# Kernel optimization log

Hardware: AMD Instinct MI355X
Metric: run time of the kernel (lower is better)

## Reference

```python
import jax, jax.numpy as jnp
import numpy as np

B, N, D_IN, D_OUT, E = 2, 50000, 128, 64, 800000
NEG_SLOPE = 0.2  # LeakyReLU negative slope (alpha)


def setup_inputs() -> dict:
    key = jax.random.key(0)
    ks = jax.random.split(key, 8)
    X_key = jax.random.normal(ks[0], (B, N, D_IN), dtype=jnp.float32)
    X_value = jax.random.normal(ks[1], (B, N, D_IN), dtype=jnp.float32)
    src = jax.random.randint(ks[2], (E,), 0, N, dtype=jnp.int32)
    dst = jnp.sort(jax.random.randint(ks[3], (E,), 0, N, dtype=jnp.int32))
    s = 1.0 / np.sqrt(D_IN)
    Wk = jax.random.normal(ks[4], (D_IN, D_OUT), dtype=jnp.float32) * s
    bk = jnp.zeros((D_OUT,), dtype=jnp.float32)
    Wv = jax.random.normal(ks[5], (D_IN, D_OUT), dtype=jnp.float32) * s
    bv = jnp.zeros((D_OUT,), dtype=jnp.float32)
    return {"X_key": X_key, "X_value": X_value, "Wk": Wk, "bk": bk,
            "Wv": Wv, "bv": bv, "src": src, "dst": dst}


def reference(X_key, X_value, Wk, bk, Wv, bv, src, dst):
    n = X_key.shape[1]
    h_key = X_key @ Wk + bk      # [B, N, D_OUT]
    h_value = X_value @ Wv + bv  # [B, N, D_OUT]

    def per_batch(hk, hv):
        # per-edge dot-product attention score
        e = jnp.sum(hk[src] * hk[dst], axis=-1)                    # [E]
        m = jax.lax.stop_gradient(jax.ops.segment_max(e, dst, num_segments=n))
        a = jnp.exp(e - m[dst])                                    # [E]
        denom = jax.ops.segment_sum(a, dst, num_segments=n)        # [N]
        num = jax.ops.segment_sum(a[:, None] * hv[src], dst, num_segments=n)  # [N, D_OUT]
        # nodes with no incoming edges get 0 (DGL leaves them zero-initialized)
        return num / jnp.where(denom == 0, 1.0, denom)[:, None]

    h_att = jax.vmap(per_batch)(h_key, h_value)  # [B, N, D_OUT]
    # LeakyReLU(alpha=0.2)
    return jnp.where(h_att >= 0, h_att, NEG_SLOPE * h_att)
```

## Files before the change

kernel.cpp:

```cpp
#include <hip/hip_runtime.h>
#include <cfloat>
#include <math.h>

#define D_IN 128
#define D_OUT 64
#define NEG_SLOPE 0.2f
#define ROWH 128
#define SQRT_LOG2E 1.2011224087864498f

typedef _Float16 half2v __attribute__((ext_vector_type(2)));
typedef _Float16 half8 __attribute__((ext_vector_type(8)));
typedef float f32x4 __attribute__((ext_vector_type(4)));

__device__ __forceinline__ unsigned short f2bf(float x) {
  union { float f; unsigned u; } a; a.f = x;
  unsigned r = a.u + 0x7FFFu + ((a.u >> 16) & 1u);
  return (unsigned short)(r >> 16);
}
__device__ __forceinline__ unsigned short f2h(float x) {
  union { _Float16 h; unsigned short u; } c;
  c.h = (_Float16)x;
  return c.u;
}
__device__ __forceinline__ float4 unpack_bf4(uint2 q) {
  union { unsigned u; float f; } t;
  float4 r;
  t.u = q.x << 16;          r.x = t.f;
  t.u = q.x & 0xFFFF0000u;  r.y = t.f;
  t.u = q.y << 16;          r.z = t.f;
  t.u = q.y & 0xFFFF0000u;  r.w = t.f;
  return r;
}
__device__ __forceinline__ float hdot4(uint2 a, uint2 b) {
  union { unsigned u; half2v h; } al, ah, bl, bh;
  al.u = a.x; ah.u = a.y; bl.u = b.x; bh.u = b.y;
#if __has_builtin(__builtin_amdgcn_fdot2)
  return __builtin_amdgcn_fdot2(al.h, bl.h,
         __builtin_amdgcn_fdot2(ah.h, bh.h, 0.f, false), false);
#else
  return (float)al.h[0] * (float)bl.h[0] + (float)al.h[1] * (float)bl.h[1] +
         (float)ah.h[0] * (float)bh.h[0] + (float)ah.h[1] * (float)bh.h[1];
#endif
}

__global__ void bfrag_kernel(const float* __restrict__ Wk,
                             const float* __restrict__ Wv,
                             _Float16* __restrict__ bfrag) {
  const int idx = blockIdx.x * 256 + threadIdx.x;
  if (idx >= 2048) return;
  const int which = idx >> 10;
  const float* __restrict__ W = which ? Wv : Wk;
  const float scale = which ? 1.0f : SQRT_LOG2E;
  const int li = idx & 1023;
  const int lane = li & 63;
  const int nt = (li >> 6) & 3;
  const int k0i = li >> 8;
  const int col = nt * 16 + (lane & 15);
  const int kbase = k0i * 32 + (lane >> 4) * 8;
  half8 h;
#pragma unroll
  for (int j = 0; j < 8; ++j)
    h[j] = (_Float16)(W[(size_t)(kbase + j) * D_OUT + col] * scale);
  reinterpret_cast<half8*>(bfrag)[idx] = h;
}

__global__ __launch_bounds__(256) void linear_mfma_kernel(
    const float* __restrict__ Xk, const float* __restrict__ Xv,
    const float* __restrict__ Wk, const float* __restrict__ bk,
    const float* __restrict__ Wv, const float* __restrict__ bv,
    const _Float16* __restrict__ bfrag, unsigned short* __restrict__ hkv,
    int R, int nblk) {
  const int which = (blockIdx.x >= nblk) ? 1 : 0;
  const int blk = blockIdx.x - which * nblk;
  const float* __restrict__ X = which ? Xv : Xk;
  const float* __restrict__ bias = which ? bv : bk;
  const float bscale = which ? 1.0f : SQRT_LOG2E;
  const int uoff = which ? D_OUT : 0;

  const int wave = threadIdx.x >> 6;
  const int lane = threadIdx.x & 63;
  const int r0 = (blk * 4 + wave) * 16;
  if (r0 >= R) return;
  const int rowi = lane & 15;
  const int kgrp = lane >> 4;

  if (r0 + 16 <= R) {
    const half8* btab =
        reinterpret_cast<const half8*>(bfrag) + (which ? 1024 : 0);
    half8 bf[4][4];
#pragma unroll
    for (int k0i = 0; k0i < 4; ++k0i)
#pragma unroll
      for (int nt = 0; nt < 4; ++nt)
        bf[k0i][nt] = btab[(k0i * 4 + nt) * 64 + lane];

    f32x4 acc[4];
#pragma unroll
    for (int nt = 0; nt < 4; ++nt) acc[nt] = (f32x4){0.f, 0.f, 0.f, 0.f};

    const float* xrow = X + (size_t)(r0 + rowi) * D_IN;
#pragma unroll
    for (int k0i = 0; k0i < 4; ++k0i) {
      const float4 x0 =
          *reinterpret_cast<const float4*>(xrow + k0i * 32 + kgrp * 8);
      const float4 x1 =
          *reinterpret_cast<const float4*>(xrow + k0i * 32 + kgrp * 8 + 4);
      half8 a;
      a[0] = (_Float16)x0.x; a[1] = (_Float16)x0.y;
      a[2] = (_Float16)x0.z; a[3] = (_Float16)x0.w;
      a[4] = (_Float16)x1.x; a[5] = (_Float16)x1.y;
      a[6] = (_Float16)x1.z; a[7] = (_Float16)x1.w;
#pragma unroll
      for (int nt = 0; nt < 4; ++nt)
        acc[nt] = __builtin_amdgcn_mfma_f32_16x16x32_f16(a, bf[k0i][nt],
                                                         acc[nt], 0, 0, 0);
    }
#pragma unroll
    for (int nt = 0; nt < 4; ++nt) {
      const int col = nt * 16 + rowi;
      const float bcol = bias[col] * bscale;
#pragma unroll
      for (int r = 0; r < 4; ++r) {
        const int row = r0 + kgrp * 4 + r;
        const float val = acc[nt][r] + bcol;
        hkv[(size_t)row * ROWH + uoff + col] =
            which ? f2bf(val) : f2h(val);
      }
    }
  } else {
    const float* __restrict__ W = which ? Wv : Wk;
    for (int r = r0; r < R; ++r) {
      const float* xr = X + (size_t)r * D_IN;
      float acc = bias[lane];
      for (int k = 0; k < D_IN; ++k)
        acc = fmaf(xr[k], W[(size_t)k * D_OUT + lane], acc);
      acc *= bscale;
      hkv[(size_t)r * ROWH + uoff + lane] = which ? f2bf(acc) : f2h(acc);
    }
  }
}

__global__ void rowptr_kernel(const int* __restrict__ dst, int E, int N,
                              int* __restrict__ row_ptr) {
  int i = blockIdx.x * blockDim.x + threadIdx.x;
  if (i > N) return;
  int lo = 0, hi = E;
  while (lo < hi) {
    int mid = (lo + hi) >> 1;
    if (dst[mid] < i) lo = mid + 1; else hi = mid;
  }
  row_ptr[i] = lo;
}

__device__ __forceinline__ float rowsum16(float p) {
  union { float f; int i; } u, v;
  u.f = p;
  v.i = __builtin_amdgcn_update_dpp(0, u.i, 0x121, 0xF, 0xF, true);
  u.f += v.f;
  v.i = __builtin_amdgcn_update_dpp(0, u.i, 0x122, 0xF, 0xF, true);
  u.f += v.f;
  v.i = __builtin_amdgcn_update_dpp(0, u.i, 0x124, 0xF, 0xF, true);
  u.f += v.f;
  v.i = __builtin_amdgcn_update_dpp(0, u.i, 0x128, 0xF, 0xF, true);
  u.f += v.f;
  return u.f;
}

struct SMState { float m, l; float4 a; };

__device__ __forceinline__ void sm_update(SMState& st, float pl,
                                          const float4& vs) {
  if (pl > st.m) {
    const float sc = exp2f(st.m - pl);
    st.l *= sc;
    st.a.x *= sc; st.a.y *= sc; st.a.z *= sc; st.a.w *= sc;
    st.m = pl;
  }
  const float a = exp2f(pl - st.m);
  st.l += a;
  st.a.x = fmaf(a, vs.x, st.a.x);
  st.a.y = fmaf(a, vs.y, st.a.y);
  st.a.z = fmaf(a, vs.z, st.a.z);
  st.a.w = fmaf(a, vs.w, st.a.w);
}

__device__ __forceinline__ void sm_merge(SMState& d, const SMState& s) {
  const float mn = fmaxf(d.m, s.m);
  const float s1 = exp2f(d.m - mn);
  const float s2 = exp2f(s.m - mn);
  d.l = d.l * s1 + s.l * s2;
  d.a.x = d.a.x * s1 + s.a.x * s2;
  d.a.y = d.a.y * s1 + s.a.y * s2;
  d.a.z = d.a.z * s1 + s.a.z * s2;
  d.a.w = d.a.w * s1 + s.a.w * s2;
  d.m = mn;
}

__device__ __forceinline__ void sm_merge_xor(SMState& d, int off) {
  SMState s;
  s.m = __shfl_xor(d.m, off, 64);
  s.l = __shfl_xor(d.l, off, 64);
  s.a.x = __shfl_xor(d.a.x, off, 64);
  s.a.y = __shfl_xor(d.a.y, off, 64);
  s.a.z = __shfl_xor(d.a.z, off, 64);
  s.a.w = __shfl_xor(d.a.w, off, 64);
  sm_merge(d, s);
}

__global__ __launch_bounds__(256) void aggregate_kernel(
    const unsigned short* __restrict__ hkv, const int* __restrict__ src,
    const int* __restrict__ row_ptr, float* __restrict__ out, int N) {
  const int node = blockIdx.x * 4 + (threadIdx.x >> 6);
  const int lane = threadIdx.x & 63;
  if (node >= N) return;
  const unsigned short* hb0 = hkv;
  const unsigned short* hb1 = hkv + (size_t)N * ROWH;

  const int li = lane & 15;
  const int g = lane >> 4;

  const uint2 kd0 = reinterpret_cast<const uint2*>(hb0 + (size_t)node * ROWH)[li];
  const uint2 kd1 = reinterpret_cast<const uint2*>(hb1 + (size_t)node * ROWH)[li];
  const int e0 = row_ptr[node];
  const int e1 = row_ptr[node + 1];

  SMState A0 = {-FLT_MAX, 0.f, {0.f, 0.f, 0.f, 0.f}};
  SMState B0 = A0, A1 = A0, B1 = A0;

  int e = e0 + g;
  for (; e + 4 < e1; e += 8) {
    const int sA = src[e];
    const int sB = src[e + 4];
    const uint2* rA0 = reinterpret_cast<const uint2*>(hb0 + (size_t)sA * ROWH);
    const uint2* rA1 = reinterpret_cast<const uint2*>(hb1 + (size_t)sA * ROWH);
    const uint2* rB0 = reinterpret_cast<const uint2*>(hb0 + (size_t)sB * ROWH);
    const uint2* rB1 = reinterpret_cast<const uint2*>(hb1 + (size_t)sB * ROWH);
    const uint2 kA0 = rA0[li], vA0 = rA0[16 + li];
    const uint2 kA1 = rA1[li], vA1 = rA1[16 + li];
    const uint2 kB0 = rB0[li], vB0 = rB0[16 + li];
    const uint2 kB1 = rB1[li], vB1 = rB1[16 + li];

    const float plA0 = rowsum16(hdot4(kA0, kd0));
    const float plA1 = rowsum16(hdot4(kA1, kd1));
    const float plB0 = rowsum16(hdot4(kB0, kd0));
    const float plB1 = rowsum16(hdot4(kB1, kd1));

    sm_update(A0, plA0, unpack_bf4(vA0));
    sm_update(A1, plA1, unpack_bf4(vA1));
    sm_update(B0, plB0, unpack_bf4(vB0));
    sm_update(B1, plB1, unpack_bf4(vB1));
  }
  if (e < e1) {
    const int sA = src[e];
    const uint2* rA0 = reinterpret_cast<const uint2*>(hb0 + (size_t)sA * ROWH);
    const uint2* rA1 = reinterpret_cast<const uint2*>(hb1 + (size_t)sA * ROWH);
    const uint2 kA0 = rA0[li], vA0 = rA0[16 + li];
    const uint2 kA1 = rA1[li], vA1 = rA1[16 + li];
    const float plA0 = rowsum16(hdot4(kA0, kd0));
    const float plA1 = rowsum16(hdot4(kA1, kd1));
    sm_update(A0, plA0, unpack_bf4(vA0));
    sm_update(A1, plA1, unpack_bf4(vA1));
  }

  sm_merge(A0, B0);
  sm_merge(A1, B1);
  sm_merge_xor(A0, 16); sm_merge_xor(A0, 32);
  sm_merge_xor(A1, 16); sm_merge_xor(A1, 32);

  if (lane < 16) {
#pragma unroll
    for (int b = 0; b < 2; ++b) {
      const SMState& S = b ? A1 : A0;
      const float denom = (S.l == 0.f) ? 1.f : S.l;
      float4 o;
      o.x = S.a.x / denom; o.y = S.a.y / denom;
      o.z = S.a.z / denom; o.w = S.a.w / denom;
      o.x = (o.x >= 0.f) ? o.x : NEG_SLOPE * o.x;
      o.y = (o.y >= 0.f) ? o.y : NEG_SLOPE * o.y;
      o.z = (o.z >= 0.f) ? o.z : NEG_SLOPE * o.z;
      o.w = (o.w >= 0.f) ? o.w : NEG_SLOPE * o.w;
      *reinterpret_cast<float4*>(out + ((size_t)b * N + node) * D_OUT + 4 * lane) = o;
    }
  }
}

extern "C" void kernel_launch(void* const* d_in, const int* in_sizes, int n_in,
                              void* d_out, int out_size, void* d_ws,
                              size_t ws_size, hipStream_t stream) {
  const float* X_key   = (const float*)d_in[0];
  const float* X_value = (const float*)d_in[1];
  const float* Wk      = (const float*)d_in[2];
  const float* bk      = (const float*)d_in[3];
  const float* Wv      = (const float*)d_in[4];
  const float* bv      = (const float*)d_in[5];
  const int*   src     = (const int*)d_in[6];
  const int*   dst     = (const int*)d_in[7];
  float* out = (float*)d_out;

  const int B = 2;
  const int R = in_sizes[0] / D_IN;
  const int N = R / B;
  const int E = in_sizes[6];

  _Float16* bfrag = (_Float16*)d_ws;
  unsigned short* hkv = (unsigned short*)((char*)d_ws + 32768);
  int* row_ptr = (int*)(hkv + (size_t)R * ROWH);

  const int blocksB = (N + 1 + 255) / 256;
  hipLaunchKernelGGL(rowptr_kernel, dim3(blocksB), dim3(256), 0, stream,
                     dst, E, N, row_ptr);
  hipLaunchKernelGGL(bfrag_kernel, dim3(8), dim3(256), 0, stream,
                     Wk, Wv, bfrag);
  const int wavesPerMat = (R + 15) / 16;
  const int nblk = (wavesPerMat + 3) / 4;
  hipLaunchKernelGGL(linear_mfma_kernel, dim3(2 * nblk), dim3(256), 0, stream,
                     X_key, X_value, Wk, bk, Wv, bv, bfrag, hkv, R, nblk);
  const int blocksC = (N + 3) / 4;
  hipLaunchKernelGGL(aggregate_kernel, dim3(blocksC), dim3(256), 0, stream,
                     hkv, src, row_ptr, out, N);
}
```

Baseline: 99.96 us.

## Map each 16-lane group to one node-batch pair with chunked softmax

The aggregation kernel now gives each 16-lane group one (node, batch) pair, so a wave covers two nodes, instead of a whole wave per node with edges split across four groups. Edges are handled in chunks of 8: all key loads and dot products are issued first, then one max and one rescale per chunk, then the value loads and accumulation. This removes the per-edge rescale branch and the cross-group shuffle merges, and keeps more loads in flight per lane. The cost is that each group walks all edges of its node serially, and the two nodes sharing a wave may have different degrees, so lanes can diverge. The src indices are also loaded twice, once per batch.

Result: slower. 127.2 us (+27.3%).

```diff
diff --git a/kernel.cpp b/kernel.cpp
--- a/kernel.cpp
+++ b/kernel.cpp
@@ -166,122 +166,70 @@
   return u.f;
 }
 
-struct SMState { float m, l; float4 a; };
-
-__device__ __forceinline__ void sm_update(SMState& st, float pl,
-                                          const float4& vs) {
-  if (pl > st.m) {
-    const float sc = exp2f(st.m - pl);
-    st.l *= sc;
-    st.a.x *= sc; st.a.y *= sc; st.a.z *= sc; st.a.w *= sc;
-    st.m = pl;
-  }
-  const float a = exp2f(pl - st.m);
-  st.l += a;
-  st.a.x = fmaf(a, vs.x, st.a.x);
-  st.a.y = fmaf(a, vs.y, st.a.y);
-  st.a.z = fmaf(a, vs.z, st.a.z);
-  st.a.w = fmaf(a, vs.w, st.a.w);
-}
-
-__device__ __forceinline__ void sm_merge(SMState& d, const SMState& s) {
-  const float mn = fmaxf(d.m, s.m);
-  const float s1 = exp2f(d.m - mn);
-  const float s2 = exp2f(s.m - mn);
-  d.l = d.l * s1 + s.l * s2;
-  d.a.x = d.a.x * s1 + s.a.x * s2;
-  d.a.y = d.a.y * s1 + s.a.y * s2;
-  d.a.z = d.a.z * s1 + s.a.z * s2;
-  d.a.w = d.a.w * s1 + s.a.w * s2;
-  d.m = mn;
-}
-
-__device__ __forceinline__ void sm_merge_xor(SMState& d, int off) {
-  SMState s;
-  s.m = __shfl_xor(d.m, off, 64);
-  s.l = __shfl_xor(d.l, off, 64);
-  s.a.x = __shfl_xor(d.a.x, off, 64);
-  s.a.y = __shfl_xor(d.a.y, off, 64);
-  s.a.z = __shfl_xor(d.a.z, off, 64);
-  s.a.w = __shfl_xor(d.a.w, off, 64);
-  sm_merge(d, s);
-}
-
 __global__ __launch_bounds__(256) void aggregate_kernel(
     const unsigned short* __restrict__ hkv, const int* __restrict__ src,
     const int* __restrict__ row_ptr, float* __restrict__ out, int N) {
-  const int node = blockIdx.x * 4 + (threadIdx.x >> 6);
+  const int wid = blockIdx.x * 4 + (threadIdx.x >> 6);
   const int lane = threadIdx.x & 63;
+  const int g = lane >> 4;
+  const int li = lane & 15;
+  const int node = wid * 2 + (g >> 1);
+  const int batch = g & 1;
   if (node >= N) return;
-  const unsigned short* hb0 = hkv;
-  const unsigned short* hb1 = hkv + (size_t)N * ROWH;
-
-  const int li = lane & 15;
-  const int g = lane >> 4;
-
-  const uint2 kd0 = reinterpret_cast<const uint2*>(hb0 + (size_t)node * ROWH)[li];
-  const uint2 kd1 = reinterpret_cast<const uint2*>(hb1 + (size_t)node * ROWH)[li];
+
+  const unsigned short* hb = hkv + (size_t)batch * N * ROWH;
+  const uint2* myrow = reinterpret_cast<const uint2*>(hb + (size_t)node * ROWH);
+  const uint2 kd = myrow[li];
   const int e0 = row_ptr[node];
   const int e1 = row_ptr[node + 1];
 
-  SMState A0 = {-FLT_MAX, 0.f, {0.f, 0.f, 0.f, 0.f}};
-  SMState B0 = A0, A1 = A0, B1 = A0;
-
-  int e = e0 + g;
-  for (; e + 4 < e1; e += 8) {
-    const int sA = src[e];
-    const int sB = src[e + 4];
-    const uint2* rA0 = reinterpret_cast<const uint2*>(hb0 + (size_t)sA * ROWH);
-    const uint2* rA1 = reinterpret_cast<const uint2*>(hb1 + (size_t)sA * ROWH);
-    const uint2* rB0 = reinterpret_cast<const uint2*>(hb0 + (size_t)sB * ROWH);
-    const uint2* rB1 = reinterpret_cast<const uint2*>(hb1 + (size_t)sB * ROWH);
-    const uint2 kA0 = rA0[li], vA0 = rA0[16 + li];
-    const uint2 kA1 = rA1[li], vA1 = rA1[16 + li];
-    const uint2 kB0 = rB0[li], vB0 = rB0[16 + li];
-    const uint2 kB1 = rB1[li], vB1 = rB1[16 + li];
-
-    const float plA0 = rowsum16(hdot4(kA0, kd0));
-    const float plA1 = rowsum16(hdot4(kA1, kd1));
-    const float plB0 = rowsum16(hdot4(kB0, kd0));
-    const float plB1 = rowsum16(hdot4(kB1, kd1));
-
-    sm_update(A0, plA0, unpack_bf4(vA0));
-    sm_update(A1, plA1, unpack_bf4(vA1));
-    sm_update(B0, plB0, unpack_bf4(vB0));
-    sm_update(B1, plB1, unpack_bf4(vB1));
+  float m = -FLT_MAX, l = 0.f;
+  float4 acc = {0.f, 0.f, 0.f, 0.f};
+
+  for (int ec = e0; ec < e1; ec += 8) {
+    int sidx[8];
+    float p[8];
+    float cmax = -FLT_MAX;
+#pragma unroll
+    for (int i = 0; i < 8; ++i) {
+      if (ec + i < e1) {
+        sidx[i] = src[ec + i];
+        const uint2 ks =
+            reinterpret_cast<const uint2*>(hb + (size_t)sidx[i] * ROWH)[li];
+        p[i] = rowsum16(hdot4(ks, kd));
+        cmax = fmaxf(cmax, p[i]);
+      }
+    }
+    const float mn = fmaxf(m, cmax);
+    const float sc = exp2f(m - mn);
+    l *= sc;
+    acc.x *= sc; acc.y *= sc; acc.z *= sc; acc.w *= sc;
+    m = mn;
+#pragma unroll
+    for (int i = 0; i < 8; ++i) {
+      if (ec + i < e1) {
+        const uint2 vu =
+            reinterpret_cast<const uint2*>(hb + (size_t)sidx[i] * ROWH)[16 + li];
+        const float a = exp2f(p[i] - m);
+        const float4 vs = unpack_bf4(vu);
+        l += a;
+        acc.x = fmaf(a, vs.x, acc.x);
+        acc.y = fmaf(a, vs.y, acc.y);
+        acc.z = fmaf(a, vs.z, acc.z);
+        acc.w = fmaf(a, vs.w, acc.w);
+      }
+    }
   }
-  if (e < e1) {
-    const int sA = src[e];
-    const uint2* rA0 = reinterpret_cast<const uint2*>(hb0 + (size_t)sA * ROWH);
-    const uint2* rA1 = reinterpret_cast<const uint2*>(hb1 + (size_t)sA * ROWH);
-    const uint2 kA0 = rA0[li], vA0 = rA0[16 + li];
-    const uint2 kA1 = rA1[li], vA1 = rA1[16 + li];
-    const float plA0 = rowsum16(hdot4(kA0, kd0));
-    const float plA1 = rowsum16(hdot4(kA1, kd1));
-    sm_update(A0, plA0, unpack_bf4(vA0));
-    sm_update(A1, plA1, unpack_bf4(vA1));
-  }
-
-  sm_merge(A0, B0);
-  sm_merge(A1, B1);
-  sm_merge_xor(A0, 16); sm_merge_xor(A0, 32);
-  sm_merge_xor(A1, 16); sm_merge_xor(A1, 32);
-
-  if (lane < 16) {
-#pragma unroll
-    for (int b = 0; b < 2; ++b) {
-      const SMState& S = b ? A1 : A0;
-      const float denom = (S.l == 0.f) ? 1.f : S.l;
-      float4 o;
-      o.x = S.a.x / denom; o.y = S.a.y / denom;
-      o.z = S.a.z / denom; o.w = S.a.w / denom;
-      o.x = (o.x >= 0.f) ? o.x : NEG_SLOPE * o.x;
-      o.y = (o.y >= 0.f) ? o.y : NEG_SLOPE * o.y;
-      o.z = (o.z >= 0.f) ? o.z : NEG_SLOPE * o.z;
-      o.w = (o.w >= 0.f) ? o.w : NEG_SLOPE * o.w;
-      *reinterpret_cast<float4*>(out + ((size_t)b * N + node) * D_OUT + 4 * lane) = o;
-    }
-  }
+
+  const float denom = (l == 0.f) ? 1.f : l;
+  float4 o;
+  o.x = acc.x / denom; o.y = acc.y / denom;
+  o.z = acc.z / denom; o.w = acc.w / denom;
+  o.x = (o.x >= 0.f) ? o.x : NEG_SLOPE * o.x;
+  o.y = (o.y >= 0.f) ? o.y : NEG_SLOPE * o.y;
+  o.z = (o.z >= 0.f) ? o.z : NEG_SLOPE * o.z;
+  o.w = (o.w >= 0.f) ? o.w : NEG_SLOPE * o.w;
+  *reinterpret_cast<float4*>(out + ((size_t)batch * N + node) * D_OUT + 4 * li) = o;
 }
 
 extern "C" void kernel_launch(void* const* d_in, const int* in_sizes, int n_in,
@@ -315,7 +263,7 @@
   const int nblk = (wavesPerMat + 3) / 4;
   hipLaunchKernelGGL(linear_mfma_kernel, dim3(2 * nblk), dim3(256), 0, stream,
                      X_key, X_value, Wk, bk, Wv, bv, bfrag, hkv, R, nblk);
-  const int blocksC = (N + 3) / 4;
+  const int blocksC = (N + 7) / 8;
   hipLaunchKernelGGL(aggregate_kernel, dim3(blocksC), dim3(256), 0, stream,
                      hkv, src, row_ptr, out, N);
 }
```

## Interleave key/value halves per row and store values as fp16 with deferred rescale

Applied to the files above, without the earlier changes.

The projection kernel now writes each node row so that every group of 4 key values is followed by the matching 4 value values. The aggregate kernel can then fetch both with a single 16-byte load per lane instead of two 8-byte loads. Values are now stored as fp16 instead of bf16, which removes the bf16 pack/unpack code. The online softmax also skips rescaling unless the new score exceeds the running max by a threshold of 8 (in log2 units). This cuts branch divergence and exp work, but lets intermediate terms grow by up to 2^8, which raises the overflow/precision risk.

Result: slower. 115.7 us (+15.7%).

```diff
diff --git a/kernel.cpp b/kernel.cpp
--- a/kernel.cpp
+++ b/kernel.cpp
@@ -7,33 +7,21 @@
 #define NEG_SLOPE 0.2f
 #define ROWH 128
 #define SQRT_LOG2E 1.2011224087864498f
+#define DEFER_THR 8.0f
 
 typedef _Float16 half2v __attribute__((ext_vector_type(2)));
 typedef _Float16 half8 __attribute__((ext_vector_type(8)));
 typedef float f32x4 __attribute__((ext_vector_type(4)));
 
-__device__ __forceinline__ unsigned short f2bf(float x) {
-  union { float f; unsigned u; } a; a.f = x;
-  unsigned r = a.u + 0x7FFFu + ((a.u >> 16) & 1u);
-  return (unsigned short)(r >> 16);
-}
 __device__ __forceinline__ unsigned short f2h(float x) {
   union { _Float16 h; unsigned short u; } c;
   c.h = (_Float16)x;
   return c.u;
 }
-__device__ __forceinline__ float4 unpack_bf4(uint2 q) {
-  union { unsigned u; float f; } t;
-  float4 r;
-  t.u = q.x << 16;          r.x = t.f;
-  t.u = q.x & 0xFFFF0000u;  r.y = t.f;
-  t.u = q.y << 16;          r.z = t.f;
-  t.u = q.y & 0xFFFF0000u;  r.w = t.f;
-  return r;
-}
-__device__ __forceinline__ float hdot4(uint2 a, uint2 b) {
+__device__ __forceinline__ float hdot4(unsigned ax, unsigned ay,
+                                       unsigned bx, unsigned by) {
   union { unsigned u; half2v h; } al, ah, bl, bh;
-  al.u = a.x; ah.u = a.y; bl.u = b.x; bh.u = b.y;
+  al.u = ax; ah.u = ay; bl.u = bx; bh.u = by;
 #if __has_builtin(__builtin_amdgcn_fdot2)
   return __builtin_amdgcn_fdot2(al.h, bl.h,
          __builtin_amdgcn_fdot2(ah.h, bh.h, 0.f, false), false);
@@ -75,7 +63,7 @@
   const float* __restrict__ X = which ? Xv : Xk;
   const float* __restrict__ bias = which ? bv : bk;
   const float bscale = which ? 1.0f : SQRT_LOG2E;
-  const int uoff = which ? D_OUT : 0;
+  const int voff = which ? 4 : 0;
 
   const int wave = threadIdx.x >> 6;
   const int lane = threadIdx.x & 63;
@@ -118,24 +106,24 @@
 #pragma unroll
     for (int nt = 0; nt < 4; ++nt) {
       const int col = nt * 16 + rowi;
+      const int uidx = 8 * (col >> 2) + (col & 3) + voff;
       const float bcol = bias[col] * bscale;
 #pragma unroll
       for (int r = 0; r < 4; ++r) {
         const int row = r0 + kgrp * 4 + r;
-        const float val = acc[nt][r] + bcol;
-        hkv[(size_t)row * ROWH + uoff + col] =
-            which ? f2bf(val) : f2h(val);
+        hkv[(size_t)row * ROWH + uidx] = f2h(acc[nt][r] + bcol);
       }
     }
   } else {
     const float* __restrict__ W = which ? Wv : Wk;
+    const int uidx = 8 * (lane >> 2) + (lane & 3) + voff;
     for (int r = r0; r < R; ++r) {
       const float* xr = X + (size_t)r * D_IN;
       float acc = bias[lane];
       for (int k = 0; k < D_IN; ++k)
         acc = fmaf(xr[k], W[(size_t)k * D_OUT + lane], acc);
       acc *= bscale;
-      hkv[(size_t)r * ROWH + uoff + lane] = which ? f2bf(acc) : f2h(acc);
+      hkv[(size_t)r * ROWH + uidx] = f2h(acc);
     }
   }
 }
@@ -169,19 +157,21 @@
 struct SMState { float m, l; float4 a; };
 
 __device__ __forceinline__ void sm_update(SMState& st, float pl,
-                                          const float4& vs) {
-  if (pl > st.m) {
+                                          const uint2& vu) {
+  if (pl > st.m + DEFER_THR) {
     const float sc = exp2f(st.m - pl);
     st.l *= sc;
     st.a.x *= sc; st.a.y *= sc; st.a.z *= sc; st.a.w *= sc;
     st.m = pl;
   }
   const float a = exp2f(pl - st.m);
+  union { unsigned u; half2v h; } vlo, vhi;
+  vlo.u = vu.x; vhi.u = vu.y;
   st.l += a;
-  st.a.x = fmaf(a, vs.x, st.a.x);
-  st.a.y = fmaf(a, vs.y, st.a.y);
-  st.a.z = fmaf(a, vs.z, st.a.z);
-  st.a.w = fmaf(a, vs.w, st.a.w);
+  st.a.x = fmaf(a, (float)vlo.h[0], st.a.x);
+  st.a.y = fmaf(a, (float)vlo.h[1], st.a.y);
+  st.a.z = fmaf(a, (float)vhi.h[0], st.a.z);
+  st.a.w = fmaf(a, (float)vhi.h[1], st.a.w);
 }
 
 __device__ __forceinline__ void sm_merge(SMState& d, const SMState& s) {
@@ -207,6 +197,14 @@
   sm_merge(d, s);
 }
 
+__device__ __forceinline__ void edge_proc(const unsigned short* __restrict__ hb,
+                                          int s, int li, const uint2& kd,
+                                          SMState& st) {
+  const uint4 q = reinterpret_cast<const uint4*>(hb + (size_t)s * ROWH)[li];
+  const float pl = rowsum16(hdot4(q.x, q.y, kd.x, kd.y));
+  sm_update(st, pl, (uint2){q.z, q.w});
+}
+
 __global__ __launch_bounds__(256) void aggregate_kernel(
     const unsigned short* __restrict__ hkv, const int* __restrict__ src,
     const int* __restrict__ row_ptr, float* __restrict__ out, int N) {
@@ -219,8 +217,10 @@
   const int li = lane & 15;
   const int g = lane >> 4;
 
-  const uint2 kd0 = reinterpret_cast<const uint2*>(hb0 + (size_t)node * ROWH)[li];
-  const uint2 kd1 = reinterpret_cast<const uint2*>(hb1 + (size_t)node * ROWH)[li];
+  const uint4 kq0 = reinterpret_cast<const uint4*>(hb0 + (size_t)node * ROWH)[li];
+  const uint4 kq1 = reinterpret_cast<const uint4*>(hb1 + (size_t)node * ROWH)[li];
+  const uint2 kd0 = {kq0.x, kq0.y};
+  const uint2 kd1 = {kq1.x, kq1.y};
   const int e0 = row_ptr[node];
   const int e1 = row_ptr[node + 1];
 
@@ -231,35 +231,15 @@
   for (; e + 4 < e1; e += 8) {
     const int sA = src[e];
     const int sB = src[e + 4];
-    const uint2* rA0 = reinterpret_cast<const uint2*>(hb0 + (size_t)sA * ROWH);
-    const uint2* rA1 = reinterpret_cast<const uint2*>(hb1 + (size_t)sA * ROWH);
-    const uint2* rB0 = reinterpret_cast<const uint2*>(hb0 + (size_t)sB * ROWH);
-    const uint2* rB1 = reinterpret_cast<const uint2*>(hb1 + (size_t)sB * ROWH);
-    const uint2 kA0 = rA0[li], vA0 = rA0[16 + li];
-    const uint2 kA1 = rA1[li], vA1 = rA1[16 + li];
-    const uint2 kB0 = rB0[li], vB0 = rB0[16 + li];
-    const uint2 kB1 = rB1[li], vB1 = rB1[16 + li];
-
-    const float plA0 = rowsum16(hdot4(kA0, kd0));
-    const float plA1 = rowsum16(hdot4(kA1, kd1));
-    const float plB0 = rowsum16(hdot4(kB0, kd0));
-    const float plB1 = rowsum16(hdot4(kB1, kd1));
-
-    sm_update(A0, plA0, unpack_bf4(vA0));
-    sm_update(A1, plA1, unpack_bf4(vA1));
-    sm_update(B0, plB0, unpack_bf4(vB0));
-    sm_update(B1, plB1, unpack_bf4(vB1));
+    edge_proc(hb0, sA, li, kd0, A0);
+    edge_proc(hb1, sA, li, kd1, A1);
+    edge_proc(hb0, sB, li, kd0, B0);
+    edge_proc(hb1, sB, li, kd1, B1);
   }
   if (e < e1) {
     const int sA = src[e];
-    const uint2* rA0 = reinterpret_cast<const uint2*>(hb0 + (size_t)sA * ROWH);
-    const uint2* rA1 = reinterpret_cast<const uint2*>(hb1 + (size_t)sA * ROWH);
-    const uint2 kA0 = rA0[li], vA0 = rA0[16 + li];
-    const uint2 kA1 = rA1[li], vA1 = rA1[16 + li];
-    const float plA0 = rowsum16(hdot4(kA0, kd0));
-    const float plA1 = rowsum16(hdot4(kA1, kd1));
-    sm_update(A0, plA0, unpack_bf4(vA0));
-    sm_update(A1, plA1, unpack_bf4(vA1));
+    edge_proc(hb0, sA, li, kd0, A0);
+    edge_proc(hb1, sA, li, kd1, A1);
   }
 
   sm_merge(A0, B0);
```
